# Optimization experiments

Measured on AMD Instinct MI355X. Metric: run time of the kernel, lower is better.

Reference implementation:

```python
import jax, jax.numpy as jnp
import numpy as np

B, N, CIN, COUT, K, L, NNZ = 4, 4096, 128, 128, 10, 50, 65536


def _spmm(idx, vals, X):
    # COO spmm: out[r] += vals * X[c]; idx: [2, nnz], X: [N, F]
    rows, cols = idx[0], idx[1]
    return jax.ops.segment_sum(vals[:, None] * X[cols], rows, num_segments=N)

_bspmm = jax.vmap(_spmm, in_axes=(0, 0, 0))  # batched over leading dim


def _hgnn_layer(phi_idx, phi_val, inv_idx, inv_val, fea, W, d):
    # original: ((phi @ diag(d)) @ phi_inv) @ (fea @ W)
    # identical math, evaluated right-to-left to stay sparse-dense only
    filt = jnp.einsum('bnc,co->bno', fea, W)            # [B,N,COUT]
    y = _bspmm(inv_idx, inv_val, filt)                  # phi_inv @ X
    y = d[None, :, None] * y                            # diag(d) @ .
    return _bspmm(phi_idx, phi_val, y)                  # phi @ .


def setup_inputs() -> dict:
    key = jax.random.key(0)
    ks = jax.random.split(key, 20)

    def coo(ki, kv):
        idx = jax.random.randint(ki, (B, 2, NNZ), 0, N, dtype=jnp.int32)
        val = jax.random.normal(kv, (B, NNZ), jnp.float32) * 0.05
        return idx, val

    phi1_idx, phi1_val = coo(ks[0], ks[1])
    phi1_inv_idx, phi1_inv_val = coo(ks[2], ks[3])
    phi2_idx, phi2_val = coo(ks[4], ks[5])
    phi2_inv_idx, phi2_inv_val = coo(ks[6], ks[7])
    fea = jax.random.normal(ks[8], (B, N, CIN), jnp.float32)
    joblst = jax.random.randint(ks[9], (B, L), 0, N, dtype=jnp.int64)

    xavier = float(np.sqrt(6.0 / (CIN + COUT)))
    W1 = jax.random.uniform(ks[10], (CIN, COUT), jnp.float32, -xavier, xavier)
    W2 = jax.random.uniform(ks[11], (CIN, COUT), jnp.float32, -xavier, xavier)
    d1 = jax.random.uniform(ks[12], (N,), jnp.float32, 0.9, 1.1)
    d2 = jax.random.uniform(ks[13], (N,), jnp.float32, 0.9, 1.1)
    s = float(1.0 / np.sqrt(N))
    W_ih = jax.random.uniform(ks[14], (N, COUT), jnp.float32, -s, s)
    W_hh = jax.random.uniform(ks[15], (N, N), jnp.float32, -s, s)
    b_ih = jax.random.uniform(ks[16], (N,), jnp.float32, -s, s)
    b_hh = jnp.zeros((N,), jnp.float32)
    sd = float(1.0 / np.sqrt(COUT))
    dense_W = jax.random.uniform(ks[17], (K, COUT), jnp.float32, -sd, sd)
    dense_b = jnp.zeros((K,), jnp.float32)
    item_emb = jax.random.normal(ks[18], (N, COUT), jnp.float32) * 0.01

    return dict(phi1_idx=phi1_idx, phi1_val=phi1_val, phi1_inv_idx=phi1_inv_idx,
                phi1_inv_val=phi1_inv_val, phi2_idx=phi2_idx, phi2_val=phi2_val,
                phi2_inv_idx=phi2_inv_idx, phi2_inv_val=phi2_inv_val,
                fea=fea, joblst=joblst, W1=W1, d1=d1, W2=W2, d2=d2,
                W_ih=W_ih, W_hh=W_hh, b_ih=b_ih, b_hh=b_hh,
                dense_W=dense_W, dense_b=dense_b, item_emb=item_emb)


def reference(phi1_idx, phi1_val, phi1_inv_idx, phi1_inv_val,
              phi2_idx, phi2_val, phi2_inv_idx, phi2_inv_val,
              fea, joblst, W1, d1, W2, d2, W_ih, W_hh, b_ih, b_hh,
              dense_W, dense_b, item_emb):
    # two hypergraph conv layers, summed
    out1 = _hgnn_layer(phi1_idx, phi1_val, phi1_inv_idx, phi1_inv_val, fea, W1, d1)
    out2 = _hgnn_layer(phi2_idx, phi2_val, phi2_inv_idx, phi2_inv_val, fea, W2, d2)
    res = out1 + out2                                   # [B,N,COUT]

    # RNN over job history embeddings (all joblst entries valid -> no -1 filter)
    xs = jnp.swapaxes(item_emb[joblst], 0, 1)           # [L,B,COUT]
    h0 = jnp.zeros((fea.shape[0], N), fea.dtype)

    def step(h, x):
        h = jnp.tanh(x @ W_ih.T + h @ W_hh.T + b_ih + b_hh)
        return h, None

    Emb, _ = jax.lax.scan(step, h0, xs)                 # last hidden: [B,N]

    res2 = jax.nn.gelu(jnp.einsum('bno,ko->bnk', res, dense_W) + dense_b,
                       approximate=False)               # [B,N,K]
    # (res3 * Emb2).permute back == res2 * gelu(Emb) broadcast over K
    return jax.nn.sigmoid(res2 * jax.nn.gelu(Emb, approximate=False)[:, :, None])
```

## Files before the change

kernel.cpp:

```cpp
#include <hip/hip_runtime.h>
#include <cstdint>
#include <cstddef>

#define NN   4096
#define LLC  50

__device__ __forceinline__ float bf2f(unsigned short u) {
    return __uint_as_float(((unsigned)u) << 16);
}
__device__ __forceinline__ unsigned short f2bf(float x) {
    unsigned b = __float_as_uint(x);
    return (unsigned short)((b + 0x7fffu + ((b >> 16) & 1u)) >> 16);
}

#if __has_builtin(__builtin_amdgcn_sdot4)
#define SDOT4(a, b, c) __builtin_amdgcn_sdot4((int)(a), (int)(b), (c), false)
#else
__device__ __forceinline__ int sdot4_sw(unsigned a, unsigned b, int c) {
    c += (int)(signed char)(a) * (int)(signed char)(b);
    c += (int)(signed char)(a >> 8) * (int)(signed char)(b >> 8);
    c += (int)(signed char)(a >> 16) * (int)(signed char)(b >> 16);
    c += (int)(signed char)(a >> 24) * (int)(signed char)(b >> 24);
    return c;
}
#define SDOT4(a, b, c) sdot4_sw((a), (b), (c))
#endif

#define DPPADD(v, ctrl, rmask) \
    ((v) + __builtin_amdgcn_update_dpp(0, (v), (ctrl), (rmask), 0xf, true))
__device__ __forceinline__ int wred64(int v) {
    v = DPPADD(v, 0x111, 0xf);
    v = DPPADD(v, 0x112, 0xf);
    v = DPPADD(v, 0x114, 0xf);
    v = DPPADD(v, 0x118, 0xf);
    v = DPPADD(v, 0x142, 0xa);
    v = DPPADD(v, 0x143, 0xc);
    return v;
}

__global__ __launch_bounds__(256) void k_xproj(const float* __restrict__ item_emb,
                                               const int* __restrict__ joblst,
                                               const float* __restrict__ W_ih,
                                               const float* __restrict__ b_ih,
                                               const float* __restrict__ b_hh,
                                               float* __restrict__ xp) {
    __shared__ float sx[8][128];
    int t = threadIdx.x;
    int n = blockIdx.x * 256 + t;
    int p0 = blockIdx.y * 8;
#pragma unroll
    for (int i = 0; i < 4; ++i) {
        int e2 = t + i * 256;
        int rr = e2 >> 7, c = e2 & 127;
        int p = p0 + rr;
        int b = p & 3, l = p >> 2;
        int j = joblst[b * LLC + l];
        sx[rr][c] = item_emb[(size_t)j * 128 + c];
    }
    __syncthreads();
    float acc[8];
#pragma unroll
    for (int r = 0; r < 8; ++r) acc[r] = 0.f;
    const float* wn = W_ih + (size_t)n * 128;
    for (int c = 0; c < 128; c += 4) {
        float4 w = *(const float4*)(wn + c);
#pragma unroll
        for (int r = 0; r < 8; ++r) {
            float4 xr = *(const float4*)&sx[r][c];
            acc[r] += xr.x * w.x + xr.y * w.y + xr.z * w.z + xr.w * w.w;
        }
    }
    float bias = b_ih[n] + b_hh[n];
#pragma unroll
    for (int r = 0; r < 8; ++r) xp[(size_t)(p0 + r) * NN + n] = acc[r] + bias;
}

__device__ __forceinline__ void row_acc(const unsigned* __restrict__ eps, int e0, int e1,
                                        const unsigned* __restrict__ Xd, unsigned bbase,
                                        unsigned lane, float& a0, float& a1) {
    int e = e0;
    for (; e + 8 <= e1; e += 8) {
        unsigned p[8], x[8];
#pragma unroll
        for (int i = 0; i < 8; ++i) p[i] = eps[e + i];
#pragma unroll
        for (int i = 0; i < 8; ++i)
            x[i] = Xd[((size_t)(bbase + (p[i] >> 16)) << 6) + lane];
#pragma unroll
        for (int i = 0; i < 8; ++i) {
            float v = bf2f((unsigned short)p[i]);
            a0 += v * bf2f((unsigned short)x[i]);
            a1 += v * bf2f((unsigned short)(x[i] >> 16));
        }
    }
    for (; e < e1; ++e) {
        unsigned pp = eps[e];
        unsigned xw = Xd[((size_t)(bbase + (pp >> 16)) << 6) + lane];
        float v = bf2f((unsigned short)pp);
        a0 += v * bf2f((unsigned short)xw);
        a1 += v * bf2f((unsigned short)(xw >> 16));
    }
}

#define WBAR(IDX)                                                              \
    __syncthreads();                                                           \
    if (t == 0) {                                                              \
        __builtin_amdgcn_fence(__ATOMIC_RELEASE, "agent");                     \
        __hip_atomic_fetch_add(&bar[IDX], 1, __ATOMIC_RELAXED,                 \
                               __HIP_MEMORY_SCOPE_AGENT);                      \
        while (__hip_atomic_load(&bar[IDX], __ATOMIC_RELAXED,                  \
                                 __HIP_MEMORY_SCOPE_AGENT) < 512)              \
            __builtin_amdgcn_s_sleep(4);                                       \
        __builtin_amdgcn_fence(__ATOMIC_ACQUIRE, "agent");                     \
    }                                                                          \
    __syncthreads();

__global__ __launch_bounds__(256, 2) void k_mega(
        const float* __restrict__ W_hh,
        const float* __restrict__ xp,
        unsigned* __restrict__ hq,
        float* __restrict__ hfin,
        int* __restrict__ bar,
        int* __restrict__ rowptr,
        unsigned* __restrict__ ep,
        unsigned short* __restrict__ filt1,
        unsigned short* __restrict__ filt2,
        unsigned short* __restrict__ y1,
        unsigned short* __restrict__ y2,
        const float* __restrict__ dW,
        const float* __restrict__ db,
        float* __restrict__ g1,
        const float* __restrict__ fea,
        const float* __restrict__ W1,
        const float* __restrict__ W2,
        const int* __restrict__ i0, const int* __restrict__ i1,
        const int* __restrict__ i2, const int* __restrict__ i3,
        const float* __restrict__ v0, const float* __restrict__ v1,
        const float* __restrict__ v2, const float* __restrict__ v3,
        const float* __restrict__ dd1, const float* __restrict__ dd2,
        int* __restrict__ counts,
        int* __restrict__ cursor) {
    __shared__ unsigned hs[4352];
    __shared__ int red[4][16];
    __shared__ unsigned char hpk[4][4][4];
    int t = threadIdx.x;
    int lane = t & 63, wv = t >> 6;
    int blk = blockIdx.x;

    if (blk >= 256) {
        int w = blk - 256;
        int c7 = w & 7;
        {
            int* lc = (int*)hs;
#pragma unroll
            for (int i = 0; i < 16; ++i) lc[t + i * 256] = 0;
            __syncthreads();
            unsigned s = (unsigned)w >> 5, ch = (unsigned)w & 31;
            unsigned m = s >> 2, b = s & 3;
            const int* ip = (m == 0) ? i0 : (m == 1) ? i1 : (m == 2) ? i2 : i3;
            unsigned base = b * 131072u + ch * 2048u;
#pragma unroll
            for (int i = 0; i < 8; ++i) {
                int r = ip[base + t + i * 256];
                atomicAdd(&lc[r], 1);
            }
            __syncthreads();
            int* cs = counts + s * 4096;
#pragma unroll
            for (int i = 0; i < 16; ++i) {
                int v = lc[t + i * 256];
                if (v) atomicAdd(cs + t + i * 256, v);
            }
        }
        WBAR(320)
        if (w < 16) {
            int s = w;
            int loc[16];
            int base = t * 16;
            const int* cs = counts + s * 4096;
            int run = 0;
#pragma unroll
            for (int i = 0; i < 16; ++i) { loc[i] = run; run += cs[base + i]; }
            int total = run;
            int v = total;
#pragma unroll
            for (int d = 1; d < 64; d <<= 1) { int u = __shfl_up(v, d, 64); if (lane >= d) v += u; }
            if (lane == 63) red[0][wv] = v;
            __syncthreads();
            int pre = v - total;
            for (int i = 0; i < wv; ++i) pre += red[0][i];
            int* rp = rowptr + s * 4097;
            int* cu = cursor + s * 4096;
#pragma unroll
            for (int i = 0; i < 16; ++i) { rp[base + i] = pre + loc[i]; cu[base + i] = pre + loc[i]; }
            if (t == 255) rp[4096] = pre + total;
        }
        WBAR(328)
        {
            unsigned s = (unsigned)w >> 5, ch = (unsigned)w & 31;
            unsigned m = s >> 2, b = s & 3;
            const int* ip = (m == 0) ? i0 : (m == 1) ? i1 : (m == 2) ? i2 : i3;
            const float* vp = (m == 0) ? v0 : (m == 1) ? v1 : (m == 2) ? v2 : v3;
            int* cu = cursor + s * 4096;
#pragma unroll
            for (int i = 0; i < 8; ++i) {
                unsigned e = ch * 2048u + i * 256u + t;
                int r = ip[(size_t)b * 131072 + e];
                int c = ip[(size_t)b * 131072 + 65536 + e];
                float v = vp[(size_t)b * 65536 + e];
                if (m == 1) v *= dd1[c];
                if (m == 3) v *= dd2[c];
                int pos = atomicAdd(cu + r, 1);
                ep[(size_t)s * 65536 + pos] = ((unsigned)c << 16) | (unsigned)f2bf(v);
            }
        }
        {
            int rb = w * 32;
            float* sfea = (float*)hs;
#pragma unroll
            for (int i = 0; i < 16; ++i) {
                int idx = t + i * 256;
                sfea[idx] = fea[(size_t)rb * 128 + idx];
            }
            __syncthreads();
            int half = t >> 7, tc = t & 127;
            const float* sf = sfea + half * (16 * 128);
            float a1[16], a2[16];
#pragma unroll
            for (int r = 0; r < 16; ++r) { a1[r] = 0.f; a2[r] = 0.f; }
            for (int c = 0; c < 128; c += 4) {
                float w10 = W1[(c + 0) * 128 + tc], w11 = W1[(c + 1) * 128 + tc];
                float w12 = W1[(c + 2) * 128 + tc], w13 = W1[(c + 3) * 128 + tc];
                float w20 = W2[(c + 0) * 128 + tc], w21 = W2[(c + 1) * 128 + tc];
                float w22 = W2[(c + 2) * 128 + tc], w23 = W2[(c + 3) * 128 + tc];
#pragma unroll
                for (int r = 0; r < 16; ++r) {
                    float4 f = *(const float4*)&sf[r * 128 + c];
                    a1[r] += f.x * w10 + f.y * w11 + f.z * w12 + f.w * w13;
                    a2[r] += f.x * w20 + f.y * w21 + f.z * w22 + f.w * w23;
                }
            }
#pragma unroll
            for (int r = 0; r < 16; ++r) {
                size_t o = (size_t)(rb + half * 16 + r) * 128 + tc;
                filt1[o] = f2bf(a1[r]);
                filt2[o] = f2bf(a2[r]);
            }
        }
        WBAR(336)
        {
            unsigned mm = c7 & 1, b = (unsigned)c7 >> 1;
            int s = (mm ? 8 : 0) + (int)b;
            const unsigned* Xd = (const unsigned*)(mm ? filt2 : filt1);
            unsigned* Yd = (unsigned*)(mm ? y2 : y1);
            const int* rp = rowptr + s * 4097;
            const unsigned* eps = ep + (size_t)s * 65536;
            unsigned bbase = b * 4096;
            int g = w >> 3;
            int row0 = (g * 4 + wv) * 16;
            for (int rr = 0; rr < 16; ++rr) {
                int row = row0 + rr;
                float a0 = 0.f, a1 = 0.f;
                row_acc(eps, rp[row], rp[row + 1], Xd, bbase, lane, a0, a1);
                Yd[((size_t)(bbase + row) << 6) + lane] =
                    (unsigned)f2bf(a0) | ((unsigned)f2bf(a1) << 16);
            }
        }
        WBAR(344)
        {
            unsigned b = (unsigned)c7 >> 1;
            unsigned bbase = b * 4096;
            const int* rpA = rowptr + (4 + (int)b) * 4097;
            const int* rpB = rowptr + (12 + (int)b) * 4097;
            const unsigned* epA = ep + (size_t)(4 + b) * 65536;
            const unsigned* epB = ep + (size_t)(12 + b) * 65536;
            const unsigned* y1d = (const unsigned*)y1;
            const unsigned* y2d = (const unsigned*)y2;
            int g2 = (w >> 3) * 2 + (w & 1);
            int row0 = (g2 * 4 + wv) * 8;
            float* fs = (float*)hs + wv * 1056;
            for (int rr = 0; rr < 8; ++rr) {
                int row = row0 + rr;
                float a0 = 0.f, a1 = 0.f;
                row_acc(epA, rpA[row], rpA[row + 1], y1d, bbase, lane, a0, a1);
                row_acc(epB, rpB[row], rpB[row + 1], y2d, bbase, lane, a0, a1);
                *(float2*)(fs + rr * 132 + 2 * lane) = make_float2(a0, a1);
            }
#pragma unroll
            for (int pass = 0; pass < 2; ++pass) {
                int task = lane + pass * 64;
                if (task < 80) {
                    int rr = task / 10, k = task - rr * 10;
                    const float* rrp = fs + rr * 132;
                    const float4* wk4 = (const float4*)(dW + (size_t)k * 128);
                    float acc = 0.f;
#pragma unroll
                    for (int c4 = 0; c4 < 32; ++c4) {
                        float4 a = *(const float4*)(rrp + c4 * 4);
                        float4 wq = wk4[c4];
                        acc += a.x * wq.x + a.y * wq.y + a.z * wq.z + a.w * wq.w;
                    }
                    float pre = acc + db[k];
                    float gg = 0.5f * pre * (1.f + erff(pre * 0.70710678118f));
                    g1[(size_t)(bbase + row0 + rr) * 10 + k] = gg;
                }
            }
        }
        return;
    }

    int row_base = ((blk & 7) * 32 + (blk >> 3)) * 16;
    int wrow = row_base + wv * 4;

    uint4 W[4][4];
    {
        const float* wsrc = W_hh + (size_t)wrow * 4096;
#pragma unroll
        for (int r = 0; r < 4; ++r)
#pragma unroll
            for (int k4 = 0; k4 < 4; ++k4) {
                unsigned q[4];
#pragma unroll
                for (int i = 0; i < 4; ++i) {
                    const float* p = wsrc + (size_t)r * 4096 + (lane * 16 + k4 * 4 + i) * 4;
                    float4 w = *(const float4*)p;
                    int q0 = (int)rintf(fminf(fmaxf(w.x * 8192.f, -127.f), 127.f));
                    int q1 = (int)rintf(fminf(fmaxf(w.y * 8192.f, -127.f), 127.f));
                    int q2 = (int)rintf(fminf(fmaxf(w.z * 8192.f, -127.f), 127.f));
                    int q3 = (int)rintf(fminf(fmaxf(w.w * 8192.f, -127.f), 127.f));
                    q[i] = (q0 & 0xff) | ((q1 & 0xff) << 8) | ((q2 & 0xff) << 16) | ((q3 & 0xff) << 24);
                }
                W[r][k4] = make_uint4(q[0], q[1], q[2], q[3]);
            }
    }

    const float SC = 1.f / (8192.f * 127.f);

    for (int l = 0; l < LLC; ++l) {
        if (l > 0) {
            const unsigned* src = hq + (size_t)((l - 1) & 1) * 4096;
            unsigned sval[16];
#pragma unroll
            for (int k = 0; k < 16; ++k)
                sval[k] = __hip_atomic_load(src + t + k * 256, __ATOMIC_RELAXED,
                                            __HIP_MEMORY_SCOPE_AGENT);
#pragma unroll
            for (int k = 0; k < 16; ++k) hs[t + k * 256] = sval[k];
            __syncthreads();

            __builtin_amdgcn_s_setprio(1);
            uint4 H[4][4];
#pragma unroll
            for (int b = 0; b < 4; ++b)
#pragma unroll
                for (int k4 = 0; k4 < 4; ++k4)
                    H[b][k4] = ((const uint4*)hs)[k4 * 256 + b * 64 + lane];
            int acc[4][4];
#pragma unroll
            for (int r = 0; r < 4; ++r)
#pragma unroll
                for (int b = 0; b < 4; ++b) acc[r][b] = 0;
#pragma unroll
            for (int k4 = 0; k4 < 4; ++k4)
#pragma unroll
                for (int r = 0; r < 4; ++r)
#pragma unroll
                    for (int b = 0; b < 4; ++b) {
                        acc[r][b] = SDOT4(W[r][k4].x, H[b][k4].x, acc[r][b]);
                        acc[r][b] = SDOT4(W[r][k4].y, H[b][k4].y, acc[r][b]);
                        acc[r][b] = SDOT4(W[r][k4].z, H[b][k4].z, acc[r][b]);
                        acc[r][b] = SDOT4(W[r][k4].w, H[b][k4].w, acc[r][b]);
                    }
#pragma unroll
            for (int r = 0; r < 4; ++r)
#pragma unroll
                for (int b = 0; b < 4; ++b) acc[r][b] = wred64(acc[r][b]);
            if (lane == 63) {
#pragma unroll
                for (int b = 0; b < 4; ++b) {
                    int4 q = { acc[0][b], acc[1][b], acc[2][b], acc[3][b] };
                    *(int4*)&red[wv][b * 4] = q;
                }
            }
            __builtin_amdgcn_s_setprio(0);
        }
        if (lane < 16) {
            int b = lane >> 2, rr = lane & 3;
            int row = wrow + rr;
            float a = (l > 0) ? (float)red[wv][lane] * SC : 0.f;
            float pre = a + xp[(size_t)(l * 4 + b) * NN + row];
            float hnew = tanhf(pre);
            if (l == LLC - 1) hfin[(size_t)b * NN + row] = hnew;
            int q = (int)rintf(hnew * 127.f);
            hpk[wv][b][rr] = (unsigned char)(q & 0xff);
        }
        if (l < LLC - 1) {
            if (lane < 4) {
                int b = lane;
                unsigned d = *(const unsigned*)&hpk[wv][b][0];
                int hk = (row_base >> 2) + wv;
                int phys = ((hk >> 2) & 3) * 1024 + b * 256 + (hk >> 4) * 4 + (hk & 3);
                __hip_atomic_store(hq + (size_t)(l & 1) * 4096 + phys, d,
                                   __ATOMIC_RELAXED, __HIP_MEMORY_SCOPE_AGENT);
            }
            __syncthreads();
            if (t == 0) {
                int g = blk & 7;
                int old = __hip_atomic_fetch_add(&bar[g * 32], 1, __ATOMIC_RELAXED,
                                                 __HIP_MEMORY_SCOPE_AGENT);
                if ((old & 31) == 31)
                    __hip_atomic_fetch_add(&bar[256], 1, __ATOMIC_RELAXED,
                                           __HIP_MEMORY_SCOPE_AGENT);
                int target = 8 * (l + 1);
                while (__hip_atomic_load(&bar[256], __ATOMIC_RELAXED,
                                         __HIP_MEMORY_SCOPE_AGENT) < target)
                    __builtin_amdgcn_s_sleep(2);
            }
            __syncthreads();
        }
    }
}

__global__ __launch_bounds__(256) void k_out(const float* __restrict__ g1,
                                             const float* __restrict__ hfin,
                                             float* __restrict__ out) {
    int i = blockIdx.x * 256 + threadIdx.x;
    int grow = i / 10;
    float e = hfin[grow];
    float ge = 0.5f * e * (1.f + erff(e * 0.70710678118f));
    out[i] = 1.f / (1.f + __expf(-g1[i] * ge));
}

extern "C" void kernel_launch(void* const* d_in, const int* in_sizes, int n_in,
                              void* d_out, int out_size, void* d_ws, size_t ws_size,
                              hipStream_t stream) {
    const int*   phi1_idx = (const int*)d_in[0];
    const float* phi1_val = (const float*)d_in[1];
    const int*   inv1_idx = (const int*)d_in[2];
    const float* inv1_val = (const float*)d_in[3];
    const int*   phi2_idx = (const int*)d_in[4];
    const float* phi2_val = (const float*)d_in[5];
    const int*   inv2_idx = (const int*)d_in[6];
    const float* inv2_val = (const float*)d_in[7];
    const float* fea      = (const float*)d_in[8];
    const int*   joblst   = (const int*)d_in[9];
    const float* W1       = (const float*)d_in[10];
    const float* d1       = (const float*)d_in[11];
    const float* W2       = (const float*)d_in[12];
    const float* d2       = (const float*)d_in[13];
    const float* W_ih     = (const float*)d_in[14];
    const float* W_hh     = (const float*)d_in[15];
    const float* b_ih     = (const float*)d_in[16];
    const float* b_hh     = (const float*)d_in[17];
    const float* dense_W  = (const float*)d_in[18];
    const float* dense_b  = (const float*)d_in[19];
    const float* item_emb = (const float*)d_in[20];

    float* ws = (float*)d_ws;
    unsigned short* filt1 = (unsigned short*)ws;
    unsigned short* filt2 = (unsigned short*)(ws + 1048576);
    unsigned short* y1    = (unsigned short*)(ws + 2097152);
    unsigned short* y2    = (unsigned short*)(ws + 3145728);
    float* g1   = ws + 4194304;
    float* xp   = ws + 6291456;
    float* hfin = ws + 7110656;
    unsigned* hq  = (unsigned*)(ws + 7127040);
    int*   counts = (int*)(ws + 11329536);
    int*   rowptr = (int*)(ws + 11395072);
    int*   cursor = (int*)(ws + 11460624);
    unsigned* ep  = (unsigned*)(ws + 11526160);
    int*   bar    = (int*)(ws + 12574736);

    hipMemsetAsync(counts, 0, 16 * 4096 * sizeof(int), stream);
    hipMemsetAsync(bar, 0, 2048, stream);

    k_xproj<<<dim3(16, 25), 256, 0, stream>>>(item_emb, joblst, W_ih, b_ih, b_hh, xp);

    k_mega<<<768, 256, 0, stream>>>(W_hh, xp, hq, hfin, bar,
                                    rowptr, ep, filt1, filt2, y1, y2,
                                    dense_W, dense_b, g1,
                                    fea, W1, W2,
                                    inv1_idx, phi1_idx, inv2_idx, phi2_idx,
                                    inv1_val, phi1_val, inv2_val, phi2_val,
                                    d1, d2, counts, cursor);

    k_out<<<640, 256, 0, stream>>>(g1, hfin, (float*)d_out);
}
```

Measured before the change: 616.7 us.

## Move sparse CSR build, feature GEMM and input projection into a separate prep kernel

```diff
diff --git a/kernel.cpp b/kernel.cpp
--- a/kernel.cpp
+++ b/kernel.cpp
@@ -38,71 +38,7 @@
     return v;
 }
 
-__global__ __launch_bounds__(256) void k_xproj(const float* __restrict__ item_emb,
-                                               const int* __restrict__ joblst,
-                                               const float* __restrict__ W_ih,
-                                               const float* __restrict__ b_ih,
-                                               const float* __restrict__ b_hh,
-                                               float* __restrict__ xp) {
-    __shared__ float sx[8][128];
-    int t = threadIdx.x;
-    int n = blockIdx.x * 256 + t;
-    int p0 = blockIdx.y * 8;
-#pragma unroll
-    for (int i = 0; i < 4; ++i) {
-        int e2 = t + i * 256;
-        int rr = e2 >> 7, c = e2 & 127;
-        int p = p0 + rr;
-        int b = p & 3, l = p >> 2;
-        int j = joblst[b * LLC + l];
-        sx[rr][c] = item_emb[(size_t)j * 128 + c];
-    }
-    __syncthreads();
-    float acc[8];
-#pragma unroll
-    for (int r = 0; r < 8; ++r) acc[r] = 0.f;
-    const float* wn = W_ih + (size_t)n * 128;
-    for (int c = 0; c < 128; c += 4) {
-        float4 w = *(const float4*)(wn + c);
-#pragma unroll
-        for (int r = 0; r < 8; ++r) {
-            float4 xr = *(const float4*)&sx[r][c];
-            acc[r] += xr.x * w.x + xr.y * w.y + xr.z * w.z + xr.w * w.w;
-        }
-    }
-    float bias = b_ih[n] + b_hh[n];
-#pragma unroll
-    for (int r = 0; r < 8; ++r) xp[(size_t)(p0 + r) * NN + n] = acc[r] + bias;
-}
-
-__device__ __forceinline__ void row_acc(const unsigned* __restrict__ eps, int e0, int e1,
-                                        const unsigned* __restrict__ Xd, unsigned bbase,
-                                        unsigned lane, float& a0, float& a1) {
-    int e = e0;
-    for (; e + 8 <= e1; e += 8) {
-        unsigned p[8], x[8];
-#pragma unroll
-        for (int i = 0; i < 8; ++i) p[i] = eps[e + i];
-#pragma unroll
-        for (int i = 0; i < 8; ++i)
-            x[i] = Xd[((size_t)(bbase + (p[i] >> 16)) << 6) + lane];
-#pragma unroll
-        for (int i = 0; i < 8; ++i) {
-            float v = bf2f((unsigned short)p[i]);
-            a0 += v * bf2f((unsigned short)x[i]);
-            a1 += v * bf2f((unsigned short)(x[i] >> 16));
-        }
-    }
-    for (; e < e1; ++e) {
-        unsigned pp = eps[e];
-        unsigned xw = Xd[((size_t)(bbase + (pp >> 16)) << 6) + lane];
-        float v = bf2f((unsigned short)pp);
-        a0 += v * bf2f((unsigned short)xw);
-        a1 += v * bf2f((unsigned short)(xw >> 16));
-    }
-}
-
-#define WBAR(IDX)                                                              \
+#define PBAR(IDX)                                                              \
     __syncthreads();                                                           \
     if (t == 0) {                                                              \
         __builtin_amdgcn_fence(__ATOMIC_RELEASE, "agent");                     \
@@ -115,31 +51,200 @@
     }                                                                          \
     __syncthreads();
 
+__global__ __launch_bounds__(256, 2) void k_prep(
+        const int* __restrict__ i0, const int* __restrict__ i1,
+        const int* __restrict__ i2, const int* __restrict__ i3,
+        const float* __restrict__ v0, const float* __restrict__ v1,
+        const float* __restrict__ v2, const float* __restrict__ v3,
+        const float* __restrict__ dd1, const float* __restrict__ dd2,
+        const float* __restrict__ fea,
+        const float* __restrict__ W1, const float* __restrict__ W2,
+        const float* __restrict__ item_emb, const int* __restrict__ joblst,
+        const float* __restrict__ W_ih,
+        const float* __restrict__ b_ih, const float* __restrict__ b_hh,
+        int* __restrict__ counts, int* __restrict__ rowptr,
+        int* __restrict__ cursor, unsigned* __restrict__ ep,
+        unsigned short* __restrict__ filt1, unsigned short* __restrict__ filt2,
+        float* __restrict__ xp, int* __restrict__ bar) {
+    __shared__ float smem[4096];
+    __shared__ int wt4[4];
+    int t = threadIdx.x;
+    int lane = t & 63, wv = t >> 6;
+    int w = blockIdx.x;
+
+    if (t < 128) counts[w * 128 + t] = 0;
+    PBAR(352)
+    {
+        int* lc = (int*)smem;
+#pragma unroll
+        for (int i = 0; i < 16; ++i) lc[t + i * 256] = 0;
+        __syncthreads();
+        unsigned s = (unsigned)w >> 5, ch = (unsigned)w & 31;
+        unsigned m = s >> 2, b = s & 3;
+        const int* ip = (m == 0) ? i0 : (m == 1) ? i1 : (m == 2) ? i2 : i3;
+        unsigned base = b * 131072u + ch * 2048u;
+#pragma unroll
+        for (int i = 0; i < 8; ++i) {
+            int r = ip[base + t + i * 256];
+            atomicAdd(&lc[r], 1);
+        }
+        __syncthreads();
+        int* cs = counts + s * 4096;
+#pragma unroll
+        for (int i = 0; i < 16; ++i) {
+            int v = lc[t + i * 256];
+            if (v) atomicAdd(cs + t + i * 256, v);
+        }
+    }
+    PBAR(360)
+    if (w < 16) {
+        int s = w;
+        int loc[16];
+        int base = t * 16;
+        const int* cs = counts + s * 4096;
+        int run = 0;
+#pragma unroll
+        for (int i = 0; i < 16; ++i) { loc[i] = run; run += cs[base + i]; }
+        int total = run;
+        int v = total;
+#pragma unroll
+        for (int d = 1; d < 64; d <<= 1) { int u = __shfl_up(v, d, 64); if (lane >= d) v += u; }
+        if (lane == 63) wt4[wv] = v;
+        __syncthreads();
+        int pre = v - total;
+        for (int i = 0; i < wv; ++i) pre += wt4[i];
+        int* rp = rowptr + s * 4097;
+        int* cu = cursor + s * 4096;
+#pragma unroll
+        for (int i = 0; i < 16; ++i) { rp[base + i] = pre + loc[i]; cu[base + i] = pre + loc[i]; }
+        if (t == 255) rp[4096] = pre + total;
+    }
+    PBAR(368)
+    if (w < 128) {
+        unsigned s = (unsigned)w >> 3, ch = (unsigned)w & 7;
+        unsigned m = s >> 2, b = s & 3;
+        const int* ip = (m == 0) ? i0 : (m == 1) ? i1 : (m == 2) ? i2 : i3;
+        const float* vp = (m == 0) ? v0 : (m == 1) ? v1 : (m == 2) ? v2 : v3;
+        int* cu = cursor + s * 4096;
+#pragma unroll 8
+        for (int i = 0; i < 32; ++i) {
+            unsigned e = ch * 8192u + i * 256u + t;
+            int r = ip[(size_t)b * 131072 + e];
+            int c = ip[(size_t)b * 131072 + 65536 + e];
+            float v = vp[(size_t)b * 65536 + e];
+            if (m == 1) v *= dd1[c];
+            if (m == 3) v *= dd2[c];
+            int pos = atomicAdd(cu + r, 1);
+            ep[(size_t)s * 65536 + pos] = ((unsigned)c << 16) | (unsigned)f2bf(v);
+        }
+    } else if (w < 384) {
+        int rb = (w - 128) * 64;
+        for (int st = 0; st < 2; ++st) {
+            int rbase = rb + st * 32;
+            if (st) __syncthreads();
+#pragma unroll
+            for (int i = 0; i < 16; ++i) {
+                int idx = t + i * 256;
+                smem[idx] = fea[(size_t)rbase * 128 + idx];
+            }
+            __syncthreads();
+            int half = t >> 7, tc = t & 127;
+            const float* sf = smem + half * 2048;
+            float a1[16], a2[16];
+#pragma unroll
+            for (int r = 0; r < 16; ++r) { a1[r] = 0.f; a2[r] = 0.f; }
+            for (int c = 0; c < 128; c += 4) {
+                float w10 = W1[(c + 0) * 128 + tc], w11 = W1[(c + 1) * 128 + tc];
+                float w12 = W1[(c + 2) * 128 + tc], w13 = W1[(c + 3) * 128 + tc];
+                float w20 = W2[(c + 0) * 128 + tc], w21 = W2[(c + 1) * 128 + tc];
+                float w22 = W2[(c + 2) * 128 + tc], w23 = W2[(c + 3) * 128 + tc];
+#pragma unroll
+                for (int r = 0; r < 16; ++r) {
+                    float4 f = *(const float4*)&sf[r * 128 + c];
+                    a1[r] += f.x * w10 + f.y * w11 + f.z * w12 + f.w * w13;
+                    a2[r] += f.x * w20 + f.y * w21 + f.z * w22 + f.w * w23;
+                }
+            }
+#pragma unroll
+            for (int r = 0; r < 16; ++r) {
+                size_t o = (size_t)(rbase + half * 16 + r) * 128 + tc;
+                filt1[o] = f2bf(a1[r]);
+                filt2[o] = f2bf(a2[r]);
+            }
+        }
+    } else {
+        int wx = w - 384;
+        int nb = wx & 15, pb = wx >> 4;
+        int p0 = pb * 25;
+        for (int idx = t; idx < 25 * 128; idx += 256) {
+            int rr = idx >> 7, c = idx & 127;
+            int p = p0 + rr;
+            int b = p & 3, l = p >> 2;
+            int j = joblst[b * LLC + l];
+            smem[idx] = item_emb[(size_t)j * 128 + c];
+        }
+        __syncthreads();
+        int n = nb * 256 + t;
+        float acc[25];
+#pragma unroll
+        for (int r = 0; r < 25; ++r) acc[r] = 0.f;
+        const float* wn = W_ih + (size_t)n * 128;
+        for (int c = 0; c < 128; c += 4) {
+            float4 wq = *(const float4*)(wn + c);
+#pragma unroll
+            for (int r = 0; r < 25; ++r) {
+                float4 xr = *(const float4*)&smem[r * 128 + c];
+                acc[r] += xr.x * wq.x + xr.y * wq.y + xr.z * wq.z + xr.w * wq.w;
+            }
+        }
+        float bias = b_ih[n] + b_hh[n];
+#pragma unroll
+        for (int r = 0; r < 25; ++r) xp[(size_t)(p0 + r) * NN + n] = acc[r] + bias;
+    }
+}
+
+__device__ __forceinline__ void row_acc(const unsigned* __restrict__ eps, int e0, int e1,
+                                        const unsigned* __restrict__ Xd, unsigned bbase,
+                                        unsigned lane, float& a0, float& a1) {
+    int e = e0;
+    for (; e + 8 <= e1; e += 8) {
+        unsigned p[8], x[8];
+#pragma unroll
+        for (int i = 0; i < 8; ++i) p[i] = eps[e + i];
+#pragma unroll
+        for (int i = 0; i < 8; ++i)
+            x[i] = Xd[((size_t)(bbase + (p[i] >> 16)) << 6) + lane];
+#pragma unroll
+        for (int i = 0; i < 8; ++i) {
+            float v = bf2f((unsigned short)p[i]);
+            a0 += v * bf2f((unsigned short)x[i]);
+            a1 += v * bf2f((unsigned short)(x[i] >> 16));
+        }
+    }
+    for (; e < e1; ++e) {
+        unsigned pp = eps[e];
+        unsigned xw = Xd[((size_t)(bbase + (pp >> 16)) << 6) + lane];
+        float v = bf2f((unsigned short)pp);
+        a0 += v * bf2f((unsigned short)xw);
+        a1 += v * bf2f((unsigned short)(xw >> 16));
+    }
+}
+
 __global__ __launch_bounds__(256, 2) void k_mega(
         const float* __restrict__ W_hh,
         const float* __restrict__ xp,
         unsigned* __restrict__ hq,
         float* __restrict__ hfin,
         int* __restrict__ bar,
-        int* __restrict__ rowptr,
-        unsigned* __restrict__ ep,
-        unsigned short* __restrict__ filt1,
-        unsigned short* __restrict__ filt2,
+        const int* __restrict__ rowptr,
+        const unsigned* __restrict__ ep,
+        const unsigned short* __restrict__ filt1,
+        const unsigned short* __restrict__ filt2,
         unsigned short* __restrict__ y1,
         unsigned short* __restrict__ y2,
         const float* __restrict__ dW,
         const float* __restrict__ db,
-        float* __restrict__ g1,
-        const float* __restrict__ fea,
-        const float* __restrict__ W1,
-        const float* __restrict__ W2,
-        const int* __restrict__ i0, const int* __restrict__ i1,
-        const int* __restrict__ i2, const int* __restrict__ i3,
-        const float* __restrict__ v0, const float* __restrict__ v1,
-        const float* __restrict__ v2, const float* __restrict__ v3,
-        const float* __restrict__ dd1, const float* __restrict__ dd2,
-        int* __restrict__ counts,
-        int* __restrict__ cursor) {
+        float* __restrict__ g1) {
     __shared__ unsigned hs[4352];
     __shared__ int red[4][16];
     __shared__ unsigned char hpk[4][4][4];
@@ -150,104 +255,6 @@
     if (blk >= 256) {
         int w = blk - 256;
         int c7 = w & 7;
-        {
-            int* lc = (int*)hs;
-#pragma unroll
-            for (int i = 0; i < 16; ++i) lc[t + i * 256] = 0;
-            __syncthreads();
-            unsigned s = (unsigned)w >> 5, ch = (unsigned)w & 31;
-            unsigned m = s >> 2, b = s & 3;
-            const int* ip = (m == 0) ? i0 : (m == 1) ? i1 : (m == 2) ? i2 : i3;
-            unsigned base = b * 131072u + ch * 2048u;
-#pragma unroll
-            for (int i = 0; i < 8; ++i) {
-                int r = ip[base + t + i * 256];
-                atomicAdd(&lc[r], 1);
-            }
-            __syncthreads();
-            int* cs = counts + s * 4096;
-#pragma unroll
-            for (int i = 0; i < 16; ++i) {
-                int v = lc[t + i * 256];
-                if (v) atomicAdd(cs + t + i * 256, v);
-            }
-        }
-        WBAR(320)
-        if (w < 16) {
-            int s = w;
-            int loc[16];
-            int base = t * 16;
-            const int* cs = counts + s * 4096;
-            int run = 0;
-#pragma unroll
-            for (int i = 0; i < 16; ++i) { loc[i] = run; run += cs[base + i]; }
-            int total = run;
-            int v = total;
-#pragma unroll
-            for (int d = 1; d < 64; d <<= 1) { int u = __shfl_up(v, d, 64); if (lane >= d) v += u; }
-            if (lane == 63) red[0][wv] = v;
-            __syncthreads();
-            int pre = v - total;
-            for (int i = 0; i < wv; ++i) pre += red[0][i];
-            int* rp = rowptr + s * 4097;
-            int* cu = cursor + s * 4096;
-#pragma unroll
-            for (int i = 0; i < 16; ++i) { rp[base + i] = pre + loc[i]; cu[base + i] = pre + loc[i]; }
-            if (t == 255) rp[4096] = pre + total;
-        }
-        WBAR(328)
-        {
-            unsigned s = (unsigned)w >> 5, ch = (unsigned)w & 31;
-            unsigned m = s >> 2, b = s & 3;
-            const int* ip = (m == 0) ? i0 : (m == 1) ? i1 : (m == 2) ? i2 : i3;
-            const float* vp = (m == 0) ? v0 : (m == 1) ? v1 : (m == 2) ? v2 : v3;
-            int* cu = cursor + s * 4096;
-#pragma unroll
-            for (int i = 0; i < 8; ++i) {
-                unsigned e = ch * 2048u + i * 256u + t;
-                int r = ip[(size_t)b * 131072 + e];
-                int c = ip[(size_t)b * 131072 + 65536 + e];
-                float v = vp[(size_t)b * 65536 + e];
-                if (m == 1) v *= dd1[c];
-                if (m == 3) v *= dd2[c];
-                int pos = atomicAdd(cu + r, 1);
-                ep[(size_t)s * 65536 + pos] = ((unsigned)c << 16) | (unsigned)f2bf(v);
-            }
-        }
-        {
-            int rb = w * 32;
-            float* sfea = (float*)hs;
-#pragma unroll
-            for (int i = 0; i < 16; ++i) {
-                int idx = t + i * 256;
-                sfea[idx] = fea[(size_t)rb * 128 + idx];
-            }
-            __syncthreads();
-            int half = t >> 7, tc = t & 127;
-            const float* sf = sfea + half * (16 * 128);
-            float a1[16], a2[16];
-#pragma unroll
-            for (int r = 0; r < 16; ++r) { a1[r] = 0.f; a2[r] = 0.f; }
-            for (int c = 0; c < 128; c += 4) {
-                float w10 = W1[(c + 0) * 128 + tc], w11 = W1[(c + 1) * 128 + tc];
-                float w12 = W1[(c + 2) * 128 + tc], w13 = W1[(c + 3) * 128 + tc];
-                float w20 = W2[(c + 0) * 128 + tc], w21 = W2[(c + 1) * 128 + tc];
-                float w22 = W2[(c + 2) * 128 + tc], w23 = W2[(c + 3) * 128 + tc];
-#pragma unroll
-                for (int r = 0; r < 16; ++r) {
-                    float4 f = *(const float4*)&sf[r * 128 + c];
-                    a1[r] += f.x * w10 + f.y * w11 + f.z * w12 + f.w * w13;
-                    a2[r] += f.x * w20 + f.y * w21 + f.z * w22 + f.w * w23;
-                }
-            }
-#pragma unroll
-            for (int r = 0; r < 16; ++r) {
-                size_t o = (size_t)(rb + half * 16 + r) * 128 + tc;
-                filt1[o] = f2bf(a1[r]);
-                filt2[o] = f2bf(a2[r]);
-            }
-        }
-        WBAR(336)
         {
             unsigned mm = c7 & 1, b = (unsigned)c7 >> 1;
             int s = (mm ? 8 : 0) + (int)b;
@@ -266,7 +273,17 @@
                     (unsigned)f2bf(a0) | ((unsigned)f2bf(a1) << 16);
             }
         }
-        WBAR(344)
+        __syncthreads();
+        if (t == 0) {
+            __builtin_amdgcn_fence(__ATOMIC_RELEASE, "agent");
+            __hip_atomic_fetch_add(&bar[320], 1, __ATOMIC_RELAXED,
+                                   __HIP_MEMORY_SCOPE_AGENT);
+            while (__hip_atomic_load(&bar[320], __ATOMIC_RELAXED,
+                                     __HIP_MEMORY_SCOPE_AGENT) < 512)
+                __builtin_amdgcn_s_sleep(4);
+            __builtin_amdgcn_fence(__ATOMIC_ACQUIRE, "agent");
+        }
+        __syncthreads();
         {
             unsigned b = (unsigned)c7 >> 1;
             unsigned bbase = b * 4096;
@@ -471,18 +488,18 @@
     unsigned* ep  = (unsigned*)(ws + 11526160);
     int*   bar    = (int*)(ws + 12574736);
 
-    hipMemsetAsync(counts, 0, 16 * 4096 * sizeof(int), stream);
     hipMemsetAsync(bar, 0, 2048, stream);
 
-    k_xproj<<<dim3(16, 25), 256, 0, stream>>>(item_emb, joblst, W_ih, b_ih, b_hh, xp);
+    k_prep<<<512, 256, 0, stream>>>(inv1_idx, phi1_idx, inv2_idx, phi2_idx,
+                                    inv1_val, phi1_val, inv2_val, phi2_val,
+                                    d1, d2, fea, W1, W2, item_emb, joblst,
+                                    W_ih, b_ih, b_hh,
+                                    counts, rowptr, cursor, ep,
+                                    filt1, filt2, xp, bar);
 
     k_mega<<<768, 256, 0, stream>>>(W_hh, xp, hq, hfin, bar,
                                     rowptr, ep, filt1, filt2, y1, y2,
-                                    dense_W, dense_b, g1,
-                                    fea, W1, W2,
-                                    inv1_idx, phi1_idx, inv2_idx, phi2_idx,
-                                    inv1_val, phi1_val, inv2_val, phi2_val,
-                                    d1, d2, counts, cursor);
+                                    dense_W, dense_b, g1);
 
     k_out<<<640, 256, 0, stream>>>(g1, hfin, (float*)d_out);
 }
```

Measured after the change: 588.3 us. -4.6%, faster.
